# Performance work log

Measured on AMD Instinct MI355X. Metric: run time of the kernel, lower is better.

Reference implementation:

```python
import jax, jax.numpy as jnp
import numpy as np

C1, C2, NUM_HEADS = 128, 128, 8
N, H_A, W_A = 2, 200, 200
H_B, W_B = 100, 360


def _polar_coords(fov, gh, gw, H, W):
    # Pixel-space polar sampling grid, matching torch linspace semantics.
    cx, cy = W // 2, H // 2
    t = jnp.arange(gw, dtype=jnp.float32) / (gw - 1)
    angles = -fov / 2 + fov * t                      # [gw]
    ca, sa = jnp.cos(angles), jnp.sin(angles)
    rmax = jnp.minimum(cx / jnp.abs(ca), cy / jnp.abs(sa))
    r = (jnp.arange(gh, dtype=jnp.float32) / (gh - 1))[:, None] * rmax[None, :]  # [gh,gw]
    x = jnp.clip(cx + r * ca, 0.0, W - 1.0)
    y = jnp.clip(cy - r * sa, 0.0, H - 1.0)
    return x, y


def _bilinear(bev, x, y):
    # grid_sample(mode='bilinear', align_corners=True) with in-range clamped coords.
    C, H, W = bev.shape
    x0 = jnp.floor(x); y0 = jnp.floor(y)
    wx = x - x0; wy = y - y0
    x0i = jnp.clip(x0.astype(jnp.int32), 0, W - 1)
    x1i = jnp.clip(x0i + 1, 0, W - 1)
    y0i = jnp.clip(y0.astype(jnp.int32), 0, H - 1)
    y1i = jnp.clip(y0i + 1, 0, H - 1)
    v00 = bev[:, y0i, x0i]; v01 = bev[:, y0i, x1i]
    v10 = bev[:, y1i, x0i]; v11 = bev[:, y1i, x1i]
    return v00 * (1 - wx) * (1 - wy) + v01 * wx * (1 - wy) + v10 * (1 - wx) * wy + v11 * wx * wy


def _restore(rect, fov, H, W):
    # scatter-add restore with count normalization (rrestore_bev_map).
    C, gh, gw = rect.shape
    x, y = _polar_coords(fov, gh, gw, H, W)
    xi = jnp.clip(jnp.round(x).astype(jnp.int32), 0, W - 1)
    yi = jnp.clip(jnp.round(y).astype(jnp.int32), 0, H - 1)
    idx = (yi * W + xi).reshape(-1)
    vals = rect.reshape(C, -1)
    acc = jnp.zeros((C, H * W), rect.dtype).at[:, idx].add(vals)
    cnt = jnp.zeros((H * W,), rect.dtype).at[idx].add(jnp.ones_like(idx, rect.dtype))
    cnt = jnp.where(cnt == 0, jnp.ones_like(cnt), cnt)
    return (acc / cnt).reshape(C, H, W)


def _mha(q, k, v, in_w, in_b, out_w, out_b, nheads):
    # torch.nn.MultiheadAttention (batch_first, eval mode -> dropout inactive).
    B, Lq, E = q.shape
    Lk = k.shape[1]
    hd = E // nheads
    wq, wk, wv = jnp.split(in_w, 3)
    bq, bk, bv = jnp.split(in_b, 3)
    qh = (q @ wq.T + bq).reshape(B, Lq, nheads, hd).transpose(0, 2, 1, 3)
    kh = (k @ wk.T + bk).reshape(B, Lk, nheads, hd).transpose(0, 2, 1, 3)
    vh = (v @ wv.T + bv).reshape(B, Lk, nheads, hd).transpose(0, 2, 1, 3)
    scores = jnp.einsum('bhqd,bhkd->bhqk', qh, kh) / jnp.sqrt(jnp.asarray(hd, q.dtype))
    attn = jax.nn.softmax(scores, axis=-1)
    o = jnp.einsum('bhqk,bhkd->bhqd', attn, vh).transpose(0, 2, 1, 3).reshape(B, Lq, E)
    return o @ out_w.T + out_b


def setup_inputs() -> dict:
    key = jax.random.key(0)
    ks = jax.random.split(key, 12)
    s1 = 1.0 / np.sqrt(C1)
    s2 = 1.0 / np.sqrt(C2)
    return {
        'list_a': jax.random.normal(ks[0], (N, C1, H_A, W_A), jnp.float32),
        'list_b': jax.random.normal(ks[1], (N, C2, H_B, W_B), jnp.float32),
        'fov_list': jax.random.uniform(ks[2], (N,), jnp.float32, 0.5 * np.pi, 0.9 * np.pi),
        'rots_list': jax.random.normal(ks[3], (N, 3, 3), jnp.float32),
        'trans_list': jax.random.normal(ks[4], (N, 3), jnp.float32),
        'Wq': jax.random.normal(ks[5], (C1, C1), jnp.float32) * s1,
        'bq': jnp.zeros((C1,), jnp.float32),
        'Wk': jax.random.normal(ks[6], (C1, C2), jnp.float32) * s2,
        'bk': jnp.zeros((C1,), jnp.float32),
        'Wv': jax.random.normal(ks[7], (C1, C2), jnp.float32) * s2,
        'bv': jnp.zeros((C1,), jnp.float32),
        'in_proj_w': jax.random.normal(ks[8], (3 * C1, C1), jnp.float32) * s1,
        'in_proj_b': jnp.zeros((3 * C1,), jnp.float32),
        'out_w': jax.random.normal(ks[9], (C1, C1), jnp.float32) * s1,
        'out_b': jnp.zeros((C1,), jnp.float32),
    }


def reference(list_a, list_b, fov_list, rots_list, trans_list,
              Wq, bq, Wk, bk, Wv, bv, in_proj_w, in_proj_b, out_w, out_b):
    def per_sample(a, b, fov):
        c1, h1, w1 = a.shape
        c2, h2, w2 = b.shape
        # extract rectangular (polar resample) of a onto (h1, w2) grid
        x, y = _polar_coords(fov, h1, w2, h1, w1)
        a_rect = _bilinear(a, x, y)                 # [C1, h1, w2]
        a_seq = a_rect.transpose(2, 1, 0)           # [w2, h1, C1]
        b_seq = b.transpose(2, 1, 0)                # [w2, h2, C2]
        q = a_seq @ Wq.T + bq
        k = b_seq @ Wk.T + bk
        v = b_seq @ Wv.T + bv
        o = _mha(q, k, v, in_proj_w, in_proj_b, out_w, out_b, NUM_HEADS)
        a_enh = o.transpose(2, 1, 0)                # [C1, h1, w2]
        return a + _restore(a_enh, fov, h1, w1)
    return jax.vmap(per_sample)(list_a, list_b, fov_list)
```

## Files before the change

kernel.cpp:

```cpp
#include <hip/hip_runtime.h>
#include <hip/hip_bf16.h>
#include <math.h>

#define C1N 128
#define HA 200
#define WA 200
#define HBB 100
#define WBB 360
#define GH 200
#define GW 360
#define NHD 8
#define HDD 16

typedef __attribute__((ext_vector_type(8))) short short8;
typedef __attribute__((ext_vector_type(4))) float f32x4;
typedef __attribute__((ext_vector_type(16))) float f32x16;

__device__ __forceinline__ float bf2f(unsigned short u) {
  union { unsigned int i; float f; } c; c.i = ((unsigned int)u) << 16; return c.f;
}
__device__ __forceinline__ unsigned short f2bf(float f) {
  __hip_bfloat16 h = __float2bfloat16(f);
  unsigned short u;
  __builtin_memcpy(&u, &h, sizeof(u));
  return u;
}

__device__ __forceinline__ void polar_xy(float fov, int i, int j, float& x, float& y) {
#pragma clang fp contract(off)
  float t = (float)j / 359.0f;
  float angle = -fov / 2.0f + fov * t;
  float ca = (float)cos((double)angle);
  float sa = (float)sin((double)angle);
  float rmax = fminf(100.0f / fabsf(ca), 100.0f / fabsf(sa));
  float r = ((float)i / 199.0f) * rmax;
  float xv = 100.0f + r * ca;
  float yv = 100.0f - r * sa;
  x = fminf(fmaxf(xv, 0.0f), 199.0f);
  y = fminf(fmaxf(yv, 0.0f), 199.0f);
}

__global__ void weff_k(const float* __restrict__ Wq, const float* __restrict__ Wk,
                       const float* __restrict__ Wv, const float* __restrict__ bq,
                       const float* __restrict__ bk, const float* __restrict__ bv,
                       const float* __restrict__ inw, const float* __restrict__ inb,
                       const float* __restrict__ outw, const float* __restrict__ outb,
                       __hip_bfloat16* __restrict__ Wb, float* __restrict__ beff) {
  int which = blockIdx.y;
  int o = blockIdx.x;
  int kcol = threadIdx.x;
  if (which == 3) {
    Wb[3 * 16384 + o * 128 + kcol] = __float2bfloat16(outw[o * 128 + kcol]);
    if (kcol == 0) beff[384 + o] = outb[o];
    return;
  }
  const float* Wx = (which == 0) ? Wq : ((which == 1) ? Wk : Wv);
  const float* bx = (which == 0) ? bq : ((which == 1) ? bk : bv);
  const float* wrow = inw + (which * 128 + o) * 128;
  float acc = 0.0f;
  for (int m = 0; m < 128; ++m) acc += wrow[m] * Wx[m * 128 + kcol];
  Wb[which * 16384 + o * 128 + kcol] = __float2bfloat16(acc);
  if (kcol == 0) {
    float bacc = inb[which * 128 + o];
    for (int m = 0; m < 128; ++m) bacc += wrow[m] * bx[m];
    beff[which * 128 + o] = bacc;
  }
}

__global__ __launch_bounds__(256) void transA_k(const float* __restrict__ a,
                                                __hip_bfloat16* __restrict__ aT) {
  __shared__ float tile[32][33];
  int p0 = blockIdx.x * 32, c0 = blockIdx.y * 32;
  int tp = threadIdx.x & 31, tr = threadIdx.x >> 5;
  for (int cc = tr; cc < 32; cc += 8)
    tile[cc][tp] = a[(size_t)(c0 + cc) * 40000 + p0 + tp];
  __syncthreads();
  for (int pp = tr; pp < 32; pp += 8)
    aT[(size_t)(p0 + pp) * C1N + c0 + tp] = __float2bfloat16(tile[tp][pp]);
}

__global__ __launch_bounds__(256) void bilinear2_k(const __hip_bfloat16* __restrict__ aT,
                                                   const float* __restrict__ fovp, int n,
                                                   __hip_bfloat16* __restrict__ aseq) {
  __shared__ float sw[20][4];
  __shared__ int sp[20][4];
  int j = blockIdx.x;
  int i_base = blockIdx.y * 20;
  int t = threadIdx.x;
  if (t < 20) {
    float x, y;
    polar_xy(fovp[n], i_base + t, j, x, y);
    float x0f = floorf(x), y0f = floorf(y);
    float wx = x - x0f, wy = y - y0f;
    int x0 = max(0, min(199, (int)x0f));
    int x1 = min(x0 + 1, 199);
    int y0 = max(0, min(199, (int)y0f));
    int y1 = min(y0 + 1, 199);
    sp[t][0] = y0 * 200 + x0; sp[t][1] = y0 * 200 + x1;
    sp[t][2] = y1 * 200 + x0; sp[t][3] = y1 * 200 + x1;
    sw[t][0] = (1.0f - wx) * (1.0f - wy); sw[t][1] = wx * (1.0f - wy);
    sw[t][2] = (1.0f - wx) * wy;          sw[t][3] = wx * wy;
  }
  __syncthreads();
  int lane = t & 63, wv = t >> 6;
  for (int ii = wv; ii < 20; ii += 4) {
    int i = i_base + ii;
    float w00 = sw[ii][0], w01 = sw[ii][1], w10 = sw[ii][2], w11 = sw[ii][3];
    ushort2 u00 = ((const ushort2*)(aT + (size_t)sp[ii][0] * C1N))[lane];
    ushort2 u01 = ((const ushort2*)(aT + (size_t)sp[ii][1] * C1N))[lane];
    ushort2 u10 = ((const ushort2*)(aT + (size_t)sp[ii][2] * C1N))[lane];
    ushort2 u11 = ((const ushort2*)(aT + (size_t)sp[ii][3] * C1N))[lane];
    float v0 = w00 * bf2f(u00.x) + w01 * bf2f(u01.x) + w10 * bf2f(u10.x) + w11 * bf2f(u11.x);
    float v1 = w00 * bf2f(u00.y) + w01 * bf2f(u01.y) + w10 * bf2f(u10.y) + w11 * bf2f(u11.y);
    ushort2 outv; outv.x = f2bf(v0); outv.y = f2bf(v1);
    ((ushort2*)(aseq + (size_t)(j * GH + i) * C1N))[lane] = outv;
  }
}

__global__ __launch_bounds__(256) void transpose_k(const float* __restrict__ b,
                                                   __hip_bfloat16* __restrict__ bs) {
  __shared__ float tile[32][33];
  int kk = blockIdx.z;
  int j0 = blockIdx.x * 32, c0 = blockIdx.y * 32;
  int tj = threadIdx.x & 31;
  int tr = threadIdx.x >> 5;
  for (int cc = tr; cc < 32; cc += 8) {
    int gj = j0 + tj;
    tile[cc][tj] = (gj < WBB) ? b[(c0 + cc) * (HBB * WBB) + kk * WBB + gj] : 0.0f;
  }
  __syncthreads();
  for (int jj = tr; jj < 32; jj += 8) {
    int gj = j0 + jj;
    if (gj < WBB)
      bs[(size_t)(gj * HBB + kk) * C1N + c0 + (threadIdx.x & 31)] =
          __float2bfloat16(tile[threadIdx.x & 31][jj]);
  }
}

__device__ __forceinline__ void gemm16_mfma(const unsigned short* __restrict__ A,
                                            const unsigned short* __restrict__ W,
                                            int m_base, f32x4 acc[8]) {
  int lane = threadIdx.x & 63;
  int col = lane & 15, quad = lane >> 4;
#pragma unroll
  for (int nt = 0; nt < 8; ++nt) acc[nt] = (f32x4)0.0f;
#pragma unroll
  for (int s = 0; s < 4; ++s) {
    short8 aF = *(const short8*)&A[(size_t)(m_base + col) * 128 + s * 32 + quad * 8];
#pragma unroll
    for (int nt = 0; nt < 8; ++nt) {
      short8 bF = *(const short8*)&W[(size_t)(nt * 16 + col) * 128 + s * 32 + quad * 8];
      acc[nt] = __builtin_amdgcn_mfma_f32_16x16x32_bf16(aF, bF, acc[nt], 0, 0, 0);
    }
  }
}

__device__ __forceinline__ void stage_bf16(unsigned short (*tile)[136],
                                           const f32x4 acc[8],
                                           const float* __restrict__ bias) {
  int lane = threadIdx.x & 63, wv = threadIdx.x >> 6;
  int col = lane & 15, quad = lane >> 4;
#pragma unroll
  for (int nt = 0; nt < 8; ++nt) {
    float bb = bias[nt * 16 + col];
#pragma unroll
    for (int r = 0; r < 4; ++r)
      tile[wv * 16 + quad * 4 + r][nt * 16 + col] = f2bf(acc[nt][r] + bb);
  }
  __syncthreads();
}

__global__ __launch_bounds__(256) void gemm_q_k(const unsigned short* __restrict__ A,
                                                const unsigned short* __restrict__ Wb,
                                                const float* __restrict__ beff,
                                                unsigned short* __restrict__ qb) {
  __shared__ unsigned short tile[64][136];
  int m0 = blockIdx.x * 64;
  f32x4 acc[8];
  gemm16_mfma(A, Wb, m0 + (threadIdx.x >> 6) * 16, acc);
  stage_bf16(tile, acc, beff);
  for (int u = threadIdx.x; u < 1024; u += 256) {
    int rl = u >> 4, ch = (u & 15) * 8;
    *(short8*)&qb[(size_t)(m0 + rl) * 128 + ch] = *(const short8*)&tile[rl][ch];
  }
}

__global__ __launch_bounds__(256) void gemm_kv_k(const unsigned short* __restrict__ A,
                                                 const unsigned short* __restrict__ Wb,
                                                 const float* __restrict__ beff,
                                                 unsigned short* __restrict__ kb,
                                                 unsigned short* __restrict__ vT) {
  __shared__ unsigned short tile[64][136];
  int which = blockIdx.y;
  int m0 = blockIdx.x * 64;
  f32x4 acc[8];
  gemm16_mfma(A, Wb + (which ? 32768 : 16384), m0 + (threadIdx.x >> 6) * 16, acc);
  stage_bf16(tile, acc, beff + (which ? 256 : 128));
  if (which == 0) {
    for (int u = threadIdx.x; u < 1024; u += 256) {
      int rl = u >> 4, ch = (u & 15) * 8;
      int row = m0 + rl;
      if (row < 36000) {
        int jj = row / 100, key = row - jj * 100;
        *(short8*)&kb[((size_t)jj * 128 + key) * 128 + ch] = *(const short8*)&tile[rl][ch];
      }
    }
  } else {
    for (int u = threadIdx.x; u < 8192; u += 256) {
      int cc = u >> 6, kl = u & 63;
      int row = m0 + kl;
      if (row < 36000) {
        int jj = row / 100, key = row - jj * 100;
        vT[((size_t)jj * 128 + cc) * 128 + key] = tile[kl][cc];
      }
    }
  }
}

__global__ __launch_bounds__(256) void gemm_o_k(const unsigned short* __restrict__ A,
                                                const unsigned short* __restrict__ Wb,
                                                const float* __restrict__ beff,
                                                float* __restrict__ C) {
  __shared__ float tile[64][132];
  int m0 = blockIdx.x * 64;
  f32x4 acc[8];
  gemm16_mfma(A, Wb + 49152, m0 + (threadIdx.x >> 6) * 16, acc);
  {
    int lane = threadIdx.x & 63, wv = threadIdx.x >> 6;
    int col = lane & 15, quad = lane >> 4;
#pragma unroll
    for (int nt = 0; nt < 8; ++nt) {
      float bb = beff[384 + nt * 16 + col];
#pragma unroll
      for (int r = 0; r < 4; ++r)
        tile[wv * 16 + quad * 4 + r][nt * 16 + col] = acc[nt][r] + bb;
    }
  }
  __syncthreads();
  for (int u = threadIdx.x; u < 2048; u += 256) {
    int rl = u >> 5, ch = (u & 31) * 4;
    *(f32x4*)&C[(size_t)(m0 + rl) * 128 + ch] = *(const f32x4*)&tile[rl][ch];
  }
}

__global__ __launch_bounds__(512) void attn5_k(const unsigned short* __restrict__ qb,
                                               const unsigned short* __restrict__ kb,
                                               const unsigned short* __restrict__ vT,
                                               unsigned short* __restrict__ o) {
  __shared__ unsigned short Ps[8][32][120];
  __shared__ unsigned short Osh[32][136];
  int mt = blockIdx.x, j = blockIdx.y;
  int h = threadIdx.x >> 6;
  int lane = threadIdx.x & 63;
  int col = lane & 31, half = lane >> 5;

  short8 qF = *(const short8*)&qb[(size_t)(j * 200 + mt * 32 + col) * 128 + h * 16 + half * 8];
  f32x16 S[4];
#pragma unroll
  for (int nt = 0; nt < 4; ++nt) {
    short8 kF = *(const short8*)&kb[((size_t)j * 128 + nt * 32 + col) * 128 + h * 16 + half * 8];
    S[nt] = __builtin_amdgcn_mfma_f32_32x32x16_bf16(kF, qF, (f32x16)0.0f, 0, 0, 0);
  }

  float rsum = 0.0f;
#pragma unroll
  for (int nt = 0; nt < 3; ++nt)
#pragma unroll
    for (int r = 0; r < 16; ++r) {
      float e = __expf(S[nt][r] * 0.25f);
      S[nt][r] = e; rsum += e;
    }
#pragma unroll
  for (int r = 0; r < 16; ++r) {
    float e = (half == 0 && r < 4) ? __expf(S[3][r] * 0.25f) : 0.0f;
    S[3][r] = e; rsum += e;
  }
  rsum += __shfl_xor(rsum, 32, 64);
  float inv = __fdividef(1.0f, rsum);

#pragma unroll
  for (int nt = 0; nt < 4; ++nt) {
#pragma unroll
    for (int g = 0; g < 4; ++g) {
      if (nt == 3 && g >= 2) continue;
      float e0 = S[nt][4 * g + 0] * inv, e1 = S[nt][4 * g + 1] * inv;
      float e2 = S[nt][4 * g + 2] * inv, e3 = S[nt][4 * g + 3] * inv;
      unsigned int lo, hi;
      asm("v_cvt_pk_bf16_f32 %0, %1, %2" : "=v"(lo) : "v"(e0), "v"(e1));
      asm("v_cvt_pk_bf16_f32 %0, %1, %2" : "=v"(hi) : "v"(e2), "v"(e3));
      *(uint2*)&Ps[h][col][nt * 32 + 8 * g + 4 * half] = make_uint2(lo, hi);
    }
  }

  short8 ones;
#pragma unroll
  for (int i = 0; i < 8; ++i) ones[i] = (short)0x3F80;
  const unsigned short* vrow = &vT[((size_t)j * 128 + h * 16 + (col & 15)) * 128];
  f32x16 O = (f32x16)0.0f;
#pragma unroll
  for (int ks = 0; ks < 7; ++ks) {
    short8 aP = *(const short8*)&Ps[h][col][ks * 16 + half * 8];
    short8 bV = (col < 16) ? *(const short8*)&vrow[ks * 16 + half * 8] : ones;
    O = __builtin_amdgcn_mfma_f32_32x32x16_bf16(aP, bV, O, 0, 0, 0);
  }
#pragma unroll
  for (int r = 0; r < 16; ++r) {
    int row = (r & 3) + 8 * (r >> 2) + 4 * half;
    if (col < 16) Osh[row][h * 16 + col] = f2bf(O[r]);
  }
  __syncthreads();
  int rl = threadIdx.x >> 4, ch = (threadIdx.x & 15) * 8;
  int qr = mt * 32 + rl;
  if (qr < 200)
    *(short8*)&o[(size_t)(j * 200 + qr) * 128 + ch] = *(const short8*)&Osh[rl][ch];
}

__global__ __launch_bounds__(256) void scatter3_k(const float* __restrict__ aenh,
                                                  const float* __restrict__ fovp, int n,
                                                  float* __restrict__ accP,
                                                  float* __restrict__ cnt) {
  __shared__ int sidx[50];
  int j = blockIdx.x;
  int i_base = blockIdx.y * 50;
  int t = threadIdx.x;
  float fov = fovp[n];
  if (t < 50) {
    float x, y;
    polar_xy(fov, i_base + t, j, x, y);
    int xi = (int)rintf(x); xi = max(0, min(199, xi));
    int yi = (int)rintf(y); yi = max(0, min(199, yi));
    sidx[t] = yi * 200 + xi;
    atomicAdd(&cnt[yi * 200 + xi], 1.0f);
  }
  __syncthreads();
  int c = t & 127;
  int half = t >> 7;
  int i0 = half * 25;
  const float* src = aenh + ((size_t)j * GH + i_base) * C1N + c;
  int cur = sidx[i0];
  float sum = 0.0f;
#pragma unroll
  for (int ib = 0; ib < 25; ib += 5) {
    float v[5];
#pragma unroll
    for (int u = 0; u < 5; ++u) v[u] = src[(size_t)(i0 + ib + u) * C1N];
#pragma unroll
    for (int u = 0; u < 5; ++u) {
      int idx = sidx[i0 + ib + u];
      if (idx != cur) {
        atomicAdd(&accP[(size_t)cur * C1N + c], sum);
        cur = idx;
        sum = v[u];
      } else {
        sum += v[u];
      }
    }
  }
  atomicAdd(&accP[(size_t)cur * C1N + c], sum);
}

__global__ __launch_bounds__(256) void finalize2_k(const float* __restrict__ a,
                                                   const float* __restrict__ accP,
                                                   const float* __restrict__ cnt,
                                                   float* __restrict__ out) {
  __shared__ float tile[64][129];
  __shared__ float sinv[64];
  int p0 = blockIdx.x * 64;
  int t = threadIdx.x;
  if (t < 64) {
    float cv = cnt[p0 + t];
    sinv[t] = 1.0f / (cv == 0.0f ? 1.0f : cv);
  }
  for (int u = t; u < 64 * 128; u += 256) {
    int pp = u >> 7, c = u & 127;
    tile[pp][c] = accP[(size_t)(p0 + pp) * C1N + c];
  }
  __syncthreads();
  for (int u = t; u < 64 * 128; u += 256) {
    int pp = u & 63, c = u >> 6;
    int g = c * 40000 + p0 + pp;
    out[g] = a[g] + tile[pp][c] * sinv[pp];
  }
}

extern "C" void kernel_launch(void* const* d_in, const int* in_sizes, int n_in,
                              void* d_out, int out_size, void* d_ws, size_t ws_size,
                              hipStream_t stream) {
  const float* list_a = (const float*)d_in[0];
  const float* list_b = (const float*)d_in[1];
  const float* fov   = (const float*)d_in[2];
  const float* Wq    = (const float*)d_in[5];
  const float* bq    = (const float*)d_in[6];
  const float* Wk    = (const float*)d_in[7];
  const float* bk    = (const float*)d_in[8];
  const float* Wv    = (const float*)d_in[9];
  const float* bv    = (const float*)d_in[10];
  const float* inw   = (const float*)d_in[11];
  const float* inb   = (const float*)d_in[12];
  const float* outw  = (const float*)d_in[13];
  const float* outb  = (const float*)d_in[14];
  float* out = (float*)d_out;
  float* ws = (float*)d_ws;

  float* beff = ws;
  __hip_bfloat16* Wb = (__hip_bfloat16*)(ws + 512);
  float* P2 = ws + 512 + 32768;
  float* qb_f = P2 + 9216000;
  float* kb_f = qb_f + 4620288;
  float* vT_f = kb_f + 2949120;
  float* P0_f = vT_f + 2949120;
  float* P1_f = P0_f + 4620288;
  float* cnt  = P1_f + 2310144;

  unsigned short* qb = (unsigned short*)qb_f;
  unsigned short* kb = (unsigned short*)kb_f;
  unsigned short* vT = (unsigned short*)vT_f;
  __hip_bfloat16* P0 = (__hip_bfloat16*)P0_f;
  __hip_bfloat16* P1 = (__hip_bfloat16*)P1_f;
  __hip_bfloat16* aT = (__hip_bfloat16*)P2;
  float* accP = P0_f;

  weff_k<<<dim3(128, 4), 128, 0, stream>>>(Wq, Wk, Wv, bq, bk, bv, inw, inb, outw, outb, Wb, beff);

  for (int n = 0; n < 2; ++n) {
    const float* a_n = list_a + (size_t)n * C1N * HA * WA;
    const float* b_n = list_b + (size_t)n * C1N * HBB * WBB;
    float* out_n = out + (size_t)n * C1N * HA * WA;

    (void)hipMemsetAsync(cnt, 0, (size_t)HA * WA * sizeof(float), stream);

    transA_k<<<dim3(1250, 4), 256, 0, stream>>>(a_n, aT);
    bilinear2_k<<<dim3(GW, 10), 256, 0, stream>>>(aT, fov, n, P0);
    transpose_k<<<dim3(12, 4, 100), 256, 0, stream>>>(b_n, P1);
    gemm_kv_k<<<dim3(563, 2), 256, 0, stream>>>((const unsigned short*)P1,
                                                (const unsigned short*)Wb, beff, kb, vT);
    gemm_q_k<<<1125, 256, 0, stream>>>((const unsigned short*)P0,
                                       (const unsigned short*)Wb, beff, qb);
    attn5_k<<<dim3(7, GW), 512, 0, stream>>>(qb, kb, vT, (unsigned short*)P0);
    gemm_o_k<<<1125, 256, 0, stream>>>((const unsigned short*)P0,
                                       (const unsigned short*)Wb, beff, P2);
    (void)hipMemsetAsync(accP, 0, (size_t)HA * WA * C1N * sizeof(float), stream);
    scatter3_k<<<dim3(GW, 4), 256, 0, stream>>>(P2, fov, n, accP, cnt);
    finalize2_k<<<625, 256, 0, stream>>>(a_n, accP, cnt, out_n);
  }
}
```

Baseline: 540.8 us.

## Fuse output projection with scatter-add and remap attention blocks across XCDs

The output-projection GEMM now does the polar scatter-add straight from its shared-memory tile, which removes the fp32 round trip of the enhanced activations (36000x128) through global memory and one kernel launch. The attention grid becomes a linear grid whose block index is remapped so that consecutive blocks on each XCD share the same key/value column, with the aim of better L2 reuse. The accumulator buffer moves to P2 and is zeroed earlier. Segments now run 32 rows per thread in row-major m order, which may produce a different pattern of atomics.

```diff
diff --git a/kernel.cpp b/kernel.cpp
--- a/kernel.cpp
+++ b/kernel.cpp
@@ -217,39 +217,16 @@
   }
 }
 
-__global__ __launch_bounds__(256) void gemm_o_k(const unsigned short* __restrict__ A,
-                                                const unsigned short* __restrict__ Wb,
-                                                const float* __restrict__ beff,
-                                                float* __restrict__ C) {
-  __shared__ float tile[64][132];
-  int m0 = blockIdx.x * 64;
-  f32x4 acc[8];
-  gemm16_mfma(A, Wb + 49152, m0 + (threadIdx.x >> 6) * 16, acc);
-  {
-    int lane = threadIdx.x & 63, wv = threadIdx.x >> 6;
-    int col = lane & 15, quad = lane >> 4;
-#pragma unroll
-    for (int nt = 0; nt < 8; ++nt) {
-      float bb = beff[384 + nt * 16 + col];
-#pragma unroll
-      for (int r = 0; r < 4; ++r)
-        tile[wv * 16 + quad * 4 + r][nt * 16 + col] = acc[nt][r] + bb;
-    }
-  }
-  __syncthreads();
-  for (int u = threadIdx.x; u < 2048; u += 256) {
-    int rl = u >> 5, ch = (u & 31) * 4;
-    *(f32x4*)&C[(size_t)(m0 + rl) * 128 + ch] = *(const f32x4*)&tile[rl][ch];
-  }
-}
-
-__global__ __launch_bounds__(512) void attn5_k(const unsigned short* __restrict__ qb,
+__global__ __launch_bounds__(512) void attn6_k(const unsigned short* __restrict__ qb,
                                                const unsigned short* __restrict__ kb,
                                                const unsigned short* __restrict__ vT,
                                                unsigned short* __restrict__ o) {
   __shared__ unsigned short Ps[8][32][120];
   __shared__ unsigned short Osh[32][136];
-  int mt = blockIdx.x, j = blockIdx.y;
+  int d = blockIdx.x;
+  int xcd = d & 7, idx = d >> 3;
+  int j = xcd * 45 + idx % 45;
+  int mt = idx / 45;
   int h = threadIdx.x >> 6;
   int lane = threadIdx.x & 63;
   int col = lane & 31, half = lane >> 5;
@@ -315,45 +292,54 @@
     *(short8*)&o[(size_t)(j * 200 + qr) * 128 + ch] = *(const short8*)&Osh[rl][ch];
 }
 
-__global__ __launch_bounds__(256) void scatter3_k(const float* __restrict__ aenh,
-                                                  const float* __restrict__ fovp, int n,
-                                                  float* __restrict__ accP,
-                                                  float* __restrict__ cnt) {
-  __shared__ int sidx[50];
-  int j = blockIdx.x;
-  int i_base = blockIdx.y * 50;
+__global__ __launch_bounds__(256) void gemm_os_k(const unsigned short* __restrict__ A,
+                                                 const unsigned short* __restrict__ Wb,
+                                                 const float* __restrict__ beff,
+                                                 const float* __restrict__ fovp, int n,
+                                                 float* __restrict__ accP,
+                                                 float* __restrict__ cnt) {
+  __shared__ float tile[64][132];
+  __shared__ int sidx[64];
+  int m0 = blockIdx.x * 64;
   int t = threadIdx.x;
-  float fov = fovp[n];
-  if (t < 50) {
+  f32x4 acc[8];
+  gemm16_mfma(A, Wb + 49152, m0 + (t >> 6) * 16, acc);
+  if (t < 64) {
+    int m = m0 + t;
+    int j = m / 200, i = m - j * 200;
     float x, y;
-    polar_xy(fov, i_base + t, j, x, y);
+    polar_xy(fovp[n], i, j, x, y);
     int xi = (int)rintf(x); xi = max(0, min(199, xi));
     int yi = (int)rintf(y); yi = max(0, min(199, yi));
     sidx[t] = yi * 200 + xi;
     atomicAdd(&cnt[yi * 200 + xi], 1.0f);
   }
-  __syncthreads();
-  int c = t & 127;
-  int half = t >> 7;
-  int i0 = half * 25;
-  const float* src = aenh + ((size_t)j * GH + i_base) * C1N + c;
-  int cur = sidx[i0];
+  {
+    int lane = t & 63, wv = t >> 6;
+    int col = lane & 15, quad = lane >> 4;
+#pragma unroll
+    for (int nt = 0; nt < 8; ++nt) {
+      float bb = beff[384 + nt * 16 + col];
+#pragma unroll
+      for (int r = 0; r < 4; ++r)
+        tile[wv * 16 + quad * 4 + r][nt * 16 + col] = acc[nt][r] + bb;
+    }
+  }
+  __syncthreads();
+  int c = t & 127, half = t >> 7;
+  int r0 = half * 32;
+  int cur = sidx[r0];
   float sum = 0.0f;
-#pragma unroll
-  for (int ib = 0; ib < 25; ib += 5) {
-    float v[5];
-#pragma unroll
-    for (int u = 0; u < 5; ++u) v[u] = src[(size_t)(i0 + ib + u) * C1N];
-#pragma unroll
-    for (int u = 0; u < 5; ++u) {
-      int idx = sidx[i0 + ib + u];
-      if (idx != cur) {
-        atomicAdd(&accP[(size_t)cur * C1N + c], sum);
-        cur = idx;
-        sum = v[u];
-      } else {
-        sum += v[u];
-      }
+#pragma unroll 4
+  for (int r = r0; r < r0 + 32; ++r) {
+    float v = tile[r][c];
+    int idx = sidx[r];
+    if (idx != cur) {
+      atomicAdd(&accP[(size_t)cur * C1N + c], sum);
+      cur = idx;
+      sum = v;
+    } else {
+      sum += v;
     }
   }
   atomicAdd(&accP[(size_t)cur * C1N + c], sum);
@@ -418,7 +404,7 @@
   __hip_bfloat16* P0 = (__hip_bfloat16*)P0_f;
   __hip_bfloat16* P1 = (__hip_bfloat16*)P1_f;
   __hip_bfloat16* aT = (__hip_bfloat16*)P2;
-  float* accP = P0_f;
+  float* accP = P2;
 
   weff_k<<<dim3(128, 4), 128, 0, stream>>>(Wq, Wk, Wv, bq, bk, bv, inw, inb, outw, outb, Wb, beff);
 
@@ -431,16 +417,16 @@
 
     transA_k<<<dim3(1250, 4), 256, 0, stream>>>(a_n, aT);
     bilinear2_k<<<dim3(GW, 10), 256, 0, stream>>>(aT, fov, n, P0);
+    (void)hipMemsetAsync(accP, 0, (size_t)HA * WA * C1N * sizeof(float), stream);
     transpose_k<<<dim3(12, 4, 100), 256, 0, stream>>>(b_n, P1);
     gemm_kv_k<<<dim3(563, 2), 256, 0, stream>>>((const unsigned short*)P1,
                                                 (const unsigned short*)Wb, beff, kb, vT);
     gemm_q_k<<<1125, 256, 0, stream>>>((const unsigned short*)P0,
                                        (const unsigned short*)Wb, beff, qb);
-    attn5_k<<<dim3(7, GW), 512, 0, stream>>>(qb, kb, vT, (unsigned short*)P0);
-    gemm_o_k<<<1125, 256, 0, stream>>>((const unsigned short*)P0,
-                                       (const unsigned short*)Wb, beff, P2);
-    (void)hipMemsetAsync(accP, 0, (size_t)HA * WA * C1N * sizeof(float), stream);
-    scatter3_k<<<dim3(GW, 4), 256, 0, stream>>>(P2, fov, n, accP, cnt);
+    attn6_k<<<2520, 512, 0, stream>>>(qb, kb, vT, (unsigned short*)P0);
+    gemm_os_k<<<1125, 256, 0, stream>>>((const unsigned short*)P0,
+                                        (const unsigned short*)Wb, beff, fov, n,
+                                        accP, cnt);
     finalize2_k<<<625, 256, 0, stream>>>(a_n, accP, cnt, out_n);
   }
 }
```

Result: faster. 507.5 us (-6.2%).
